# Performance work log

Hardware: AMD Instinct MI355X
Metric: run time of the kernel (lower is better)

## Reference

```python
import jax, jax.numpy as jnp
import numpy as np

# Config mirroring the TF module: cross-attention path (one_on_rna == 2),
# use_attn_augument=1, aug_multiply=0, two_d_softm=1, two_d_softm_mul_row_count=1,
# reduce_level=20 (protok used for padding masks).
B, L, D, H = 4, 1024, 512, 8
DEPTH = D // H          # 64, matches the repeat(64) in padding_to_zeros
NEG = -1.0e9


def setup_inputs() -> dict:
    key = jax.random.key(0)
    ks = jax.random.split(key, 16)
    s = np.float32(1.0 / np.sqrt(D))  # glorot-ish scale
    q = jax.random.normal(ks[0], (B, L, D), jnp.float32)
    kv = jax.random.normal(ks[1], (B, L, D), jnp.float32)
    # protein tokens; 0 == padding (compared against 0.0 in the TF code)
    protok = jax.random.randint(ks[2], (B, L), 0, 21).astype(jnp.float32)
    statpot_hb = jax.random.uniform(ks[3], (B, L, L), dtype=jnp.float32)
    statpot_pi = jax.random.uniform(ks[4], (B, L, L), dtype=jnp.float32)
    # cross padding mask: 1.0 where the protein (query) position is padding
    pad = (protok == 0.0).astype(jnp.float32)            # [B, L]
    cross_mask = jnp.broadcast_to(pad[:, :, None], (B, L, L)).astype(jnp.float32)
    wq = jax.random.normal(ks[5], (D, D), jnp.float32) * s
    wk = jax.random.normal(ks[6], (D, D), jnp.float32) * s
    wv = jax.random.normal(ks[7], (D, D), jnp.float32) * s
    wo = jax.random.normal(ks[8], (D, D), jnp.float32) * s
    bq = jnp.zeros((D,), jnp.float32)
    bk = jnp.zeros((D,), jnp.float32)
    bv = jnp.zeros((D,), jnp.float32)
    bo = jnp.zeros((D,), jnp.float32)
    aug_weight_att = jnp.ones((1,), jnp.float32)
    aug_weight_aug = jnp.ones((1,), jnp.float32)
    return dict(q=q, kv=kv, protok=protok, statpot_hb=statpot_hb,
                statpot_pi=statpot_pi, cross_mask=cross_mask,
                wq=wq, bq=bq, wk=wk, bk=bk, wv=wv, bv=bv, wo=wo, bo=bo,
                aug_weight_att=aug_weight_att, aug_weight_aug=aug_weight_aug)


def _split_heads(x):
    # [B, L, D] -> [B, H, L, depth]
    return x.reshape(B, L, H, DEPTH).transpose(0, 2, 1, 3)


def reference(q, kv, protok, statpot_hb, statpot_pi, cross_mask,
              wq, bq, wk, bk, wv, bv, wo, bo, aug_weight_att, aug_weight_aug):
    # padding_to_zeros: zero features at padded protein positions
    pad_keep = (protok != 0.0).astype(q.dtype)[:, :, None]   # [B, L, 1]
    qp = (q @ wq + bq) * pad_keep   # query side is the protein (len == max_pro_len)
    k = kv @ wk + bk
    v = kv @ wv + bv
    qh, kh, vh = _split_heads(qp), _split_heads(k), _split_heads(v)

    # unscaled QK^T (original does NOT divide by sqrt(depth))
    logits = jnp.einsum('bhqd,bhkd->bhqk', qh, kh)           # [B,H,L,L]

    # statistical-potential augmentation (aug_multiply == 0 -> additive)
    table = jnp.stack([statpot_hb, statpot_pi], axis=1)      # [B,2,L,L]
    table = jnp.repeat(table, H // 2, axis=1)                # [B,H,L,L]
    logits = logits / jnp.max(logits)
    logits = aug_weight_att * logits
    table = aug_weight_aug * table
    table = table / jnp.max(table)
    logits = logits + table

    # additive large-negative mask, broadcast over heads
    logits = logits + cross_mask[:, None, :, :] * NEG

    # 2D softmax jointly over (query, key) axes
    attn = jax.nn.softmax(logits.reshape(B, H, L * L), axis=-1).reshape(B, H, L, L)

    # rescale by number of non-padded protein rows (two_d_softm_mul_row_count)
    mul = jnp.count_nonzero(protok, axis=1).astype(attn.dtype)[:, None, None, None]
    attn = attn * mul
    attn = attn / jnp.max(attn)

    # output = attn^T @ v : contracts the QUERY axis (as in the original matmul)
    out = jnp.einsum('bhqk,bhqd->bhkd', attn, vh)            # [B,H,L,depth]
    out = out.transpose(0, 2, 1, 3).reshape(B, L, D)
    out = out @ wo + bo
    out = out * pad_keep                                     # final padding zeroing
    return out
```

## Files before the change

kernel.cpp:

```cpp
#include <hip/hip_runtime.h>
#include <math.h>

#define BB 4
#define LL 1024
#define DD 512
#define HH 8
#define DEP 64
#define NEGV (-1.0e9f)

typedef __attribute__((ext_vector_type(8))) short bf16x8;
typedef __attribute__((ext_vector_type(4))) float f32x4;
typedef unsigned short u16;
typedef unsigned int u32;

#define S_TMAX 1
#define S_TMIN 2
#define S_MUL  4
#define S_SUM  8
#define S_M    40
#define P_TMAX 128
#define P_TMIN 384
#define P_GMAX 640
#define SCAL_F 1792
#define PER_T  (BB*HH*LL*DEP)

__device__ inline u16 f2b(float x) {
  u32 u = __float_as_uint(x);
  return (u16)((u + 0x7FFFu + ((u >> 16) & 1u)) >> 16);
}
__device__ inline float b2f(u16 h) { return __uint_as_float(((u32)h) << 16); }

__device__ inline void atomicMaxF(float* addr, float val) {
  unsigned int* ua = (unsigned int*)addr;
  unsigned int old = *ua;
  while (__uint_as_float(old) < val) {
    unsigned int assumed = old;
    old = atomicCAS(ua, assumed, __float_as_uint(val));
    if (old == assumed) break;
  }
}

__global__ __launch_bounds__(256) void k_tminmax(const float* __restrict__ hb,
                                                 const float* __restrict__ pi,
                                                 const float* __restrict__ protok,
                                                 float* __restrict__ ws) {
  const int t = threadIdx.x;
  if (blockIdx.x == 4 && t < 32) {
    ws[S_SUM + t] = 0.0f; ws[S_M + t] = -INFINITY;
  }
  if (blockIdx.x < 4) {
    int b = blockIdx.x;
    int cnt = 0;
    for (int l = t; l < LL; l += 256)
      cnt += (protok[b*LL + l] != 0.0f) ? 1 : 0;
    __shared__ int shc[4];
    int lane = t & 63, w = t >> 6;
    #pragma unroll
    for (int o = 32; o > 0; o >>= 1) cnt += __shfl_down(cnt, o);
    if (lane == 0) shc[w] = cnt;
    __syncthreads();
    if (t == 0) ws[S_MUL + b] = (float)(shc[0] + shc[1] + shc[2] + shc[3]);
  }
  const int g = blockIdx.x*256 + t;
  float mx = -INFINITY, mn = INFINITY;
  #pragma unroll
  for (int rep = 0; rep < 4; ++rep) {
    float4 a[4], c[4];
    #pragma unroll
    for (int j = 0; j < 4; ++j) {
      size_t idx = (size_t)rep*262144 + (size_t)j*65536 + g;
      a[j] = ((const float4*)hb)[idx];
      c[j] = ((const float4*)pi)[idx];
    }
    #pragma unroll
    for (int j = 0; j < 4; ++j) {
      mx = fmaxf(mx, fmaxf(fmaxf(a[j].x, a[j].y), fmaxf(a[j].z, a[j].w)));
      mx = fmaxf(mx, fmaxf(fmaxf(c[j].x, c[j].y), fmaxf(c[j].z, c[j].w)));
      mn = fminf(mn, fminf(fminf(a[j].x, a[j].y), fminf(a[j].z, a[j].w)));
      mn = fminf(mn, fminf(fminf(c[j].x, c[j].y), fminf(c[j].z, c[j].w)));
    }
  }
  __shared__ float shx[4], shn[4];
  int lane = t & 63, w = t >> 6;
  #pragma unroll
  for (int o = 32; o > 0; o >>= 1) {
    mx = fmaxf(mx, __shfl_down(mx, o));
    mn = fminf(mn, __shfl_down(mn, o));
  }
  if (lane == 0) { shx[w] = mx; shn[w] = mn; }
  __syncthreads();
  if (t == 0) {
    ws[P_TMAX + blockIdx.x] = fmaxf(fmaxf(shx[0], shx[1]), fmaxf(shx[2], shx[3]));
    ws[P_TMIN + blockIdx.x] = fminf(fminf(shn[0], shn[1]), fminf(shn[2], shn[3]));
  }
}

__global__ __launch_bounds__(256) void k_prep(
    const float* __restrict__ q, const float* __restrict__ kv,
    const float* __restrict__ wq, const float* __restrict__ wk,
    const float* __restrict__ wv, const float* __restrict__ wo,
    u16* __restrict__ Xb, u16* __restrict__ WTb, float* __restrict__ ws) {
  const int bid = blockIdx.x;
  const int t = threadIdx.x;
  if (bid < 2048) {
    int tg = bid*256 + t;
    int which = tg >> 18;
    size_t off8 = (size_t)(tg & 262143) * 8;
    const float* s = which ? kv : q;
    float4 f0 = *(const float4*)&s[off8];
    float4 f1 = *(const float4*)&s[off8 + 4];
    u32 p0 = (u32)f2b(f0.x) | ((u32)f2b(f0.y) << 16);
    u32 p1 = (u32)f2b(f0.z) | ((u32)f2b(f0.w) << 16);
    u32 p2 = (u32)f2b(f1.x) | ((u32)f2b(f1.y) << 16);
    u32 p3 = (u32)f2b(f1.z) | ((u32)f2b(f1.w) << 16);
    *(int4*)&Xb[(size_t)which*PER_T + off8] = make_int4(p0, p1, p2, p3);
  } else if (bid < 2304) {
    const int wid = bid - 2048;
    const int g = wid >> 6, rem = wid & 63;
    const int k0 = (rem >> 3)*64, n0 = (rem & 7)*64;
    const float* W = (g==0)?wq:(g==1)?wk:(g==2)?wv:wo;
    __shared__ u16 Ls[64][72];
    {
      const int r = t>>2, c16 = (t&3)*16;
      float v[16];
      #pragma unroll
      for (int j=0;j<4;++j) {
        float4 f = *(const float4*)&W[(size_t)(k0+r)*DD + n0 + c16 + 4*j];
        v[4*j]=f.x; v[4*j+1]=f.y; v[4*j+2]=f.z; v[4*j+3]=f.w;
      }
      u32 pk_[8];
      #pragma unroll
      for (int j=0;j<8;++j) pk_[j] = (u32)f2b(v[2*j]) | ((u32)f2b(v[2*j+1])<<16);
      *(int4*)&Ls[r][c16]   = make_int4(pk_[0],pk_[1],pk_[2],pk_[3]);
      *(int4*)&Ls[r][c16+8] = make_int4(pk_[4],pk_[5],pk_[6],pk_[7]);
    }
    __syncthreads();
    {
      const int n = t>>2, kk = (t&3)*16;
      u16 u[16];
      #pragma unroll
      for (int j=0;j<16;++j) u[j] = Ls[kk+j][n];
      u32 q_[8];
      #pragma unroll
      for (int j=0;j<8;++j) q_[j] = (u32)u[2*j] | ((u32)u[2*j+1]<<16);
      size_t dst = ((size_t)(g*DD + n0 + n))*DD + k0 + kk;
      *(int4*)&WTb[dst]   = make_int4(q_[0],q_[1],q_[2],q_[3]);
      *(int4*)&WTb[dst+8] = make_int4(q_[4],q_[5],q_[6],q_[7]);
    }
  } else {
    float tm = ws[P_TMAX + t];
    float tn = ws[P_TMIN + t];
    __shared__ float st[4], sn[4];
    int lane = t & 63, w = t >> 6;
    #pragma unroll
    for (int o = 32; o > 0; o >>= 1) {
      tm = fmaxf(tm, __shfl_down(tm, o));
      tn = fminf(tn, __shfl_down(tn, o));
    }
    if (lane == 0) { st[w] = tm; sn[w] = tn; }
    __syncthreads();
    if (t == 0) {
      ws[S_TMAX] = fmaxf(fmaxf(st[0], st[1]), fmaxf(st[2], st[3]));
      ws[S_TMIN] = fminf(fminf(sn[0], sn[1]), fminf(sn[2], sn[3]));
    }
  }
}

__global__ __launch_bounds__(256) void k1_proj(
    const float* __restrict__ protok,
    const float* __restrict__ bq, const float* __restrict__ bk,
    const float* __restrict__ bv,
    const u16* __restrict__ Xb, const u16* __restrict__ WTb,
    u16* __restrict__ QPb, u16* __restrict__ KHb, u16* __restrict__ VTb) {
  const int gid = blockIdx.z;
  const u16* X = Xb + (gid == 0 ? 0 : (size_t)PER_T);
  const float* bia = (gid == 0) ? bq : (gid == 1) ? bk : bv;
  const int m0 = blockIdx.x*64;
  const int h  = blockIdx.y;
  __shared__ u16 As[64][72];
  __shared__ u16 Bs[64][72];
  const int t = threadIdx.x;
  const int w = t>>6, lane = t&63, i = lane&15, g2 = lane>>4;
  const int sr = t>>2, sc = (t&3)*16;

  f32x4 acc[4];
  #pragma unroll
  for (int ct=0;ct<4;++ct) acc[ct] = (f32x4){0.f,0.f,0.f,0.f};

  for (int kk0 = 0; kk0 < DD; kk0 += 64) {
    __syncthreads();
    {
      size_t sx = (size_t)(m0+sr)*DD + kk0 + sc;
      *(int4*)&As[sr][sc]   = *(const int4*)&X[sx];
      *(int4*)&As[sr][sc+8] = *(const int4*)&X[sx+8];
    }
    {
      size_t src = ((size_t)(gid*DD + h*64 + sr))*DD + kk0 + sc;
      *(int4*)&Bs[sr][sc]   = *(const int4*)&WTb[src];
      *(int4*)&Bs[sr][sc+8] = *(const int4*)&WTb[src+8];
    }
    __syncthreads();
    bf16x8 a0 = *(const bf16x8*)&As[16*w + i][g2*8];
    bf16x8 a1 = *(const bf16x8*)&As[16*w + i][32 + g2*8];
    #pragma unroll
    for (int ct=0; ct<4; ++ct) {
      bf16x8 b0 = *(const bf16x8*)&Bs[ct*16 + i][g2*8];
      bf16x8 b1 = *(const bf16x8*)&Bs[ct*16 + i][32 + g2*8];
      acc[ct] = __builtin_amdgcn_mfma_f32_16x16x32_bf16(a0, b0, acc[ct], 0,0,0);
      acc[ct] = __builtin_amdgcn_mfma_f32_16x16x32_bf16(a1, b1, acc[ct], 0,0,0);
    }
  }
  __syncthreads();
  const int lrow = 16*w + g2*4;
  if (gid == 2) {
    #pragma unroll
    for (int ct=0;ct<4;++ct)
      #pragma unroll
      for (int r=0;r<4;++r)
        As[lrow + r][ct*16 + i] = f2b(acc[ct][r] + bia[h*64 + ct*16 + i]);
    __syncthreads();
    const int b = m0 >> 10, l0 = m0 & 1023;
    const int d = t>>2, lc = (t&3)*16;
    u16 u[16];
    #pragma unroll
    for (int j=0;j<16;++j) u[j] = As[lc+j][d];
    u32 q_[8];
    #pragma unroll
    for (int j=0;j<8;++j) q_[j] = (u32)u[2*j] | ((u32)u[2*j+1]<<16);
    size_t dst = ((size_t)(b*HH + h)*DEP + d)*LL + l0 + lc;
    *(int4*)&VTb[dst]   = make_int4(q_[0],q_[1],q_[2],q_[3]);
    *(int4*)&VTb[dst+8] = make_int4(q_[4],q_[5],q_[6],q_[7]);
  } else {
    u16* Y = (gid == 0) ? QPb : KHb;
    #pragma unroll
    for (int ct=0;ct<4;++ct)
      #pragma unroll
      for (int r=0;r<4;++r) {
        int m = m0 + lrow + r;
        float keep = (gid == 0) ? ((protok[m] != 0.0f) ? 1.0f : 0.0f) : 1.0f;
        int b = m >> 10, l = m & 1023;
        float val = (acc[ct][r] + bia[h*64 + ct*16 + i]) * keep;
        Y[((size_t)(b*HH + h)*LL + l)*DEP + ct*16 + i] = f2b(val);
      }
  }
}

__global__ __launch_bounds__(256) void k3_gmax(
    const u16* __restrict__ QPb, const u16* __restrict__ KHb,
    float* __restrict__ wsf) {
  const int q0 = blockIdx.x*128, bh = blockIdx.y, kz = blockIdx.z;
  __shared__ u16 Qs[2][64][72];
  __shared__ u16 Ks[2][64][72];
  const int t = threadIdx.x;
  const int w = t>>6, lane = t&63, i = lane&15, g2 = lane>>4;
  const int sr = t>>2, sc = (t&3)*16;
  const u16* Qb = QPb + (size_t)bh*LL*DEP;
  const u16* Kb = KHb + (size_t)bh*LL*DEP;
  #pragma unroll
  for (int qs = 0; qs < 2; ++qs) {
    size_t sq = (size_t)(q0 + qs*64 + sr)*DEP + sc;
    *(int4*)&Qs[qs][sr][sc]   = *(const int4*)&Qb[sq];
    *(int4*)&Qs[qs][sr][sc+8] = *(const int4*)&Qb[sq+8];
  }
  const int kb = kz*4;
  int4 rn0 = *(const int4*)&Kb[(size_t)(kb*64 + sr)*DEP + sc];
  int4 rn1 = *(const int4*)&Kb[(size_t)(kb*64 + sr)*DEP + sc + 8];
  __syncthreads();
  *(int4*)&Ks[0][sr][sc]   = rn0;
  *(int4*)&Ks[0][sr][sc+8] = rn1;
  rn0 = *(const int4*)&Kb[(size_t)((kb+1)*64 + sr)*DEP + sc];
  rn1 = *(const int4*)&Kb[(size_t)((kb+1)*64 + sr)*DEP + sc + 8];
  __syncthreads();
  bf16x8 a0[2], a1[2];
  #pragma unroll
  for (int qs = 0; qs < 2; ++qs) {
    a0[qs] = *(const bf16x8*)&Qs[qs][16*w + i][g2*8];
    a1[qs] = *(const bf16x8*)&Qs[qs][16*w + i][32 + g2*8];
  }
  float mx = -INFINITY;
  for (int kt = 0; kt < 4; ++kt) {
    const int cur = kt & 1;
    #pragma unroll
    for (int ct=0;ct<4;++ct) {
      bf16x8 b0 = *(const bf16x8*)&Ks[cur][ct*16 + i][g2*8];
      bf16x8 b1 = *(const bf16x8*)&Ks[cur][ct*16 + i][32 + g2*8];
      #pragma unroll
      for (int qs=0;qs<2;++qs) {
        f32x4 z = (f32x4){0.f,0.f,0.f,0.f};
        z = __builtin_amdgcn_mfma_f32_16x16x32_bf16(a0[qs], b0, z, 0,0,0);
        z = __builtin_amdgcn_mfma_f32_16x16x32_bf16(a1[qs], b1, z, 0,0,0);
        mx = fmaxf(mx, fmaxf(fmaxf(z[0],z[1]), fmaxf(z[2],z[3])));
      }
    }
    if (kt < 3) {
      __syncthreads();
      *(int4*)&Ks[cur^1][sr][sc]   = rn0;
      *(int4*)&Ks[cur^1][sr][sc+8] = rn1;
      if (kt < 2) {
        rn0 = *(const int4*)&Kb[(size_t)((kb+kt+2)*64 + sr)*DEP + sc];
        rn1 = *(const int4*)&Kb[(size_t)((kb+kt+2)*64 + sr)*DEP + sc + 8];
      }
      __syncthreads();
    }
  }
  __shared__ float red[4];
  #pragma unroll
  for (int o = 32; o > 0; o >>= 1) mx = fmaxf(mx, __shfl_down(mx, o));
  if (lane == 0) red[w] = mx;
  __syncthreads();
  if (t == 0)
    wsf[P_GMAX + (bh*8 + blockIdx.x)*4 + kz] =
        fmaxf(fmaxf(red[0],red[1]), fmaxf(red[2],red[3]));
}

__global__ __launch_bounds__(256) void k4_fused(
    const float* __restrict__ protok,
    const float* __restrict__ hb, const float* __restrict__ pi,
    const float* __restrict__ w_att, const float* __restrict__ w_aug,
    const u16* __restrict__ QPb, const u16* __restrict__ KHb,
    const u16* __restrict__ VTb,
    u16* __restrict__ Ob0, u16* __restrict__ Ob1,
    float* __restrict__ wsf) {
  const int k0 = blockIdx.x*64;
  const int bh = blockIdx.y, b = bh>>3, h = bh&7;
  const int qbase = blockIdx.z * 512;
  u16* Obz = blockIdx.z ? Ob1 : Ob0;
  const float* tab = ((h < 4) ? hb : pi) + (size_t)b*LL*LL;
  const int t = threadIdx.x;
  const int w = t>>6, lane = t&63, i = lane&15, g2 = lane>>4;
  const int sr = t>>2, sc = (t&3)*16;
  const int qlb = 16*w + g2*4;

  __shared__ float gsh;
  {
    float gm = -INFINITY;
    #pragma unroll
    for (int j=0;j<4;++j) gm = fmaxf(gm, wsf[P_GMAX + j*256 + t]);
    __shared__ float red[4];
    #pragma unroll
    for (int o = 32; o > 0; o >>= 1) gm = fmaxf(gm, __shfl_down(gm, o));
    if (lane == 0) red[w] = gm;
    __syncthreads();
    if (t == 0) gsh = fmaxf(fmaxf(red[0],red[1]), fmaxf(red[2],red[3]));
  }
  const float tmaxr = wsf[S_TMAX], tminr = wsf[S_TMIN];
  const float wa = w_att[0], wg = w_aug[0];
  const float tden = (wg >= 0.0f) ? (wg * tmaxr) : (wg * tminr);
  const float inv_t = wg / tden;

  __shared__ u16 Ks[64][72];
  __shared__ u16 Qs[64][72];
  __shared__ u16 Vt[64][72];
  __shared__ u16 Pt[64][72];
  {
    size_t sk = ((size_t)bh*LL + k0 + sr)*DEP + sc;
    *(int4*)&Ks[sr][sc]   = *(const int4*)&KHb[sk];
    *(int4*)&Ks[sr][sc+8] = *(const int4*)&KHb[sk+8];
  }
  int4 rq0 = *(const int4*)&QPb[((size_t)bh*LL + qbase + sr)*DEP + sc];
  int4 rq1 = *(const int4*)&QPb[((size_t)bh*LL + qbase + sr)*DEP + sc + 8];
  int4 rv0 = *(const int4*)&VTb[((size_t)bh*DEP + sr)*LL + qbase + sc];
  int4 rv1 = *(const int4*)&VTb[((size_t)bh*DEP + sr)*LL + qbase + sc + 8];
  float tvr[4][4];
  #pragma unroll
  for (int r=0;r<4;++r)
    #pragma unroll
    for (int ct=0;ct<4;++ct)
      tvr[r][ct] = tab[(size_t)(qbase + qlb + r)*LL + k0 + ct*16 + i];
  __syncthreads();
  const float inv_g = wa / gsh;
  bf16x8 kb0[4], kb1[4];
  #pragma unroll
  for (int ct=0;ct<4;++ct) {
    kb0[ct] = *(const bf16x8*)&Ks[ct*16 + i][g2*8];
    kb1[ct] = *(const bf16x8*)&Ks[ct*16 + i][32 + g2*8];
  }
  f32x4 accO[4];
  #pragma unroll
  for (int dt=0;dt<4;++dt) accO[dt] = (f32x4){0.f,0.f,0.f,0.f};
  float lsum = 0.0f, lmax = -INFINITY;

  for (int q0 = qbase; q0 < qbase + 512; q0 += 64) {
    const bool more = (q0 + 64) < (qbase + 512);
    __syncthreads();
    *(int4*)&Qs[sr][sc]   = rq0;
    *(int4*)&Qs[sr][sc+8] = rq1;
    *(int4*)&Vt[sr][sc]   = rv0;
    *(int4*)&Vt[sr][sc+8] = rv1;
    __syncthreads();
    if (more) {
      rq0 = *(const int4*)&QPb[((size_t)bh*LL + q0 + 64 + sr)*DEP + sc];
      rq1 = *(const int4*)&QPb[((size_t)bh*LL + q0 + 64 + sr)*DEP + sc + 8];
      rv0 = *(const int4*)&VTb[((size_t)bh*DEP + sr)*LL + q0 + 64 + sc];
      rv1 = *(const int4*)&VTb[((size_t)bh*DEP + sr)*LL + q0 + 64 + sc + 8];
    }
    bf16x8 a0 = *(const bf16x8*)&Qs[16*w + i][g2*8];
    bf16x8 a1 = *(const bf16x8*)&Qs[16*w + i][32 + g2*8];
    f32x4 s4[4];
    #pragma unroll
    for (int ct=0; ct<4; ++ct) {
      f32x4 z = (f32x4){0.f,0.f,0.f,0.f};
      z = __builtin_amdgcn_mfma_f32_16x16x32_bf16(a0, kb0[ct], z, 0,0,0);
      z = __builtin_amdgcn_mfma_f32_16x16x32_bf16(a1, kb1[ct], z, 0,0,0);
      s4[ct] = z;
    }
    float tv2[4][4];
    if (more) {
      #pragma unroll
      for (int r=0;r<4;++r)
        #pragma unroll
        for (int ct=0;ct<4;++ct)
          tv2[r][ct] = tab[(size_t)(q0 + 64 + qlb + r)*LL + k0 + ct*16 + i];
    }
    float madd[4];
    #pragma unroll
    for (int r=0;r<4;++r)
      madd[r] = (protok[b*LL + q0 + qlb + r] == 0.0f) ? NEGV : 0.0f;
    #pragma unroll
    for (int ct=0;ct<4;++ct) {
      float pr[4];
      #pragma unroll
      for (int r=0;r<4;++r) {
        float sp = fmaf(s4[ct][r], inv_g, fmaf(tvr[r][ct], inv_t, madd[r]));
        lmax = fmaxf(lmax, sp);
        float p = __expf(sp);
        lsum += p;
        pr[r] = p;
      }
      u32 pk0 = (u32)f2b(pr[0]) | ((u32)f2b(pr[1])<<16);
      u32 pk1 = (u32)f2b(pr[2]) | ((u32)f2b(pr[3])<<16);
      *(uint2*)&Pt[ct*16 + i][qlb] = make_uint2(pk0, pk1);
    }
    __syncthreads();
    bf16x8 pa0 = *(const bf16x8*)&Pt[16*w + i][g2*8];
    bf16x8 pa1 = *(const bf16x8*)&Pt[16*w + i][32 + g2*8];
    #pragma unroll
    for (int dt=0; dt<4; ++dt) {
      bf16x8 v0 = *(const bf16x8*)&Vt[dt*16 + i][g2*8];
      bf16x8 v1 = *(const bf16x8*)&Vt[dt*16 + i][32 + g2*8];
      accO[dt] = __builtin_amdgcn_mfma_f32_16x16x32_bf16(pa0, v0, accO[dt], 0,0,0);
      accO[dt] = __builtin_amdgcn_mfma_f32_16x16x32_bf16(pa1, v1, accO[dt], 0,0,0);
    }
    if (more) {
      #pragma unroll
      for (int r=0;r<4;++r)
        #pragma unroll
        for (int ct=0;ct<4;++ct) tvr[r][ct] = tv2[r][ct];
    }
  }
  #pragma unroll
  for (int dt=0;dt<4;++dt)
    #pragma unroll
    for (int r=0;r<4;++r)
      Obz[((size_t)bh*LL + k0 + qlb + r)*DEP + dt*16 + i] = f2b(accO[dt][r]);
  __shared__ float rs[4], rm[4];
  #pragma unroll
  for (int o = 32; o > 0; o >>= 1) {
    lsum += __shfl_down(lsum, o);
    lmax = fmaxf(lmax, __shfl_down(lmax, o));
  }
  if (lane == 0) { rs[w] = lsum; rm[w] = lmax; }
  __syncthreads();
  if (t == 0) {
    atomicAdd(&wsf[S_SUM + bh], rs[0]+rs[1]+rs[2]+rs[3]);
    atomicMaxF(&wsf[S_M + bh], fmaxf(fmaxf(rm[0], rm[1]), fmaxf(rm[2], rm[3])));
  }
}

__global__ __launch_bounds__(256) void k5_out(
    const float* __restrict__ protok,
    const float* __restrict__ bo,
    const u16* __restrict__ WTb,
    const u16* __restrict__ O0, const u16* __restrict__ O1,
    const float* __restrict__ wsf, float* __restrict__ out) {
  const int m0 = blockIdx.x*64, n0 = blockIdx.y*64;
  const int b = m0 >> 10, l0 = m0 & 1023;
  __shared__ u16 As[64][72];
  __shared__ u16 Bs[64][72];
  __shared__ float csh[8];
  const int t = threadIdx.x;
  const int w = t>>6, lane = t&63, i = lane&15, g2 = lane>>4;
  const int sr = t>>2, sc = (t&3)*16;

  __shared__ float ash[32];
  if (t < 32)
    ash[t] = wsf[S_MUL + (t>>3)] * __expf(wsf[S_M + t]) / wsf[S_SUM + t];
  __syncthreads();
  if (t < 8) {
    float amax = -INFINITY;
    #pragma unroll
    for (int j = 0; j < 32; ++j) amax = fmaxf(amax, ash[j]);
    csh[t] = (wsf[S_MUL + b] / wsf[S_SUM + b*HH + t]) / amax;
  }

  f32x4 acc[4];
  #pragma unroll
  for (int ct=0;ct<4;++ct) acc[ct] = (f32x4){0.f,0.f,0.f,0.f};

  for (int kk0 = 0; kk0 < DD; kk0 += 64) {
    const int h = kk0 >> 6;
    __syncthreads();
    {
      union { int4 v[2]; u16 u[16]; } u0, u1;
      size_t so = ((size_t)(b*HH + h)*LL + l0 + sr)*DEP + sc;
      u0.v[0] = *(const int4*)&O0[so];
      u0.v[1] = *(const int4*)&O0[so+8];
      u1.v[0] = *(const int4*)&O1[so];
      u1.v[1] = *(const int4*)&O1[so+8];
      const float cs = csh[h];
      u32 pk_[8];
      #pragma unroll
      for (int j=0;j<8;++j) {
        float lo = (b2f(u0.u[2*j])   + b2f(u1.u[2*j]))   * cs;
        float hi = (b2f(u0.u[2*j+1]) + b2f(u1.u[2*j+1])) * cs;
        pk_[j] = (u32)f2b(lo) | ((u32)f2b(hi)<<16);
      }
      *(int4*)&As[sr][sc]   = make_int4(pk_[0],pk_[1],pk_[2],pk_[3]);
      *(int4*)&As[sr][sc+8] = make_int4(pk_[4],pk_[5],pk_[6],pk_[7]);
    }
    {
      size_t src = ((size_t)(3*DD + n0 + sr))*DD + kk0 + sc;
      *(int4*)&Bs[sr][sc]   = *(const int4*)&WTb[src];
      *(int4*)&Bs[sr][sc+8] = *(const int4*)&WTb[src+8];
    }
    __syncthreads();
    bf16x8 a0 = *(const bf16x8*)&As[16*w + i][g2*8];
    bf16x8 a1 = *(const bf16x8*)&As[16*w + i][32 + g2*8];
    #pragma unroll
    for (int ct=0; ct<4; ++ct) {
      bf16x8 b0 = *(const bf16x8*)&Bs[ct*16 + i][g2*8];
      bf16x8 b1 = *(const bf16x8*)&Bs[ct*16 + i][32 + g2*8];
      acc[ct] = __builtin_amdgcn_mfma_f32_16x16x32_bf16(a0, b0, acc[ct], 0,0,0);
      acc[ct] = __builtin_amdgcn_mfma_f32_16x16x32_bf16(a1, b1, acc[ct], 0,0,0);
    }
  }
  #pragma unroll
  for (int ct=0;ct<4;++ct)
    #pragma unroll
    for (int r=0;r<4;++r) {
      int m = m0 + 16*w + g2*4 + r;
      float keep = (protok[m] != 0.0f) ? 1.0f : 0.0f;
      out[(size_t)m*DD + n0 + ct*16 + i] = (acc[ct][r] + bo[n0 + ct*16 + i]) * keep;
    }
}

extern "C" void kernel_launch(void* const* d_in, const int* in_sizes, int n_in,
                              void* d_out, int out_size, void* d_ws, size_t ws_size,
                              hipStream_t stream) {
  const float* q      = (const float*)d_in[0];
  const float* kv     = (const float*)d_in[1];
  const float* protok = (const float*)d_in[2];
  const float* hb     = (const float*)d_in[3];
  const float* pi     = (const float*)d_in[4];
  const float* wq = (const float*)d_in[6];
  const float* bq = (const float*)d_in[7];
  const float* wk = (const float*)d_in[8];
  const float* bk = (const float*)d_in[9];
  const float* wv = (const float*)d_in[10];
  const float* bv = (const float*)d_in[11];
  const float* wo = (const float*)d_in[12];
  const float* bo = (const float*)d_in[13];
  const float* w_att = (const float*)d_in[14];
  const float* w_aug = (const float*)d_in[15];
  float* wsf = (float*)d_ws;
  float* out = (float*)d_out;

  u16* base = (u16*)(wsf + SCAL_F);
  u16* QPb = base;
  u16* KHb = QPb + PER_T;
  u16* VTb = KHb + PER_T;
  u16* XO  = VTb + PER_T;
  u16* WTb = XO  + 2*PER_T;
  u16* Xb  = XO;
  u16* Ob0 = XO;
  u16* Ob1 = XO + PER_T;

  k_tminmax <<<256, 256, 0, stream>>>(hb, pi, protok, wsf);
  k_prep    <<<2305, 256, 0, stream>>>(q, kv, wq, wk, wv, wo, Xb, WTb, wsf);
  k1_proj   <<<dim3(64, 8, 3), 256, 0, stream>>>(protok, bq, bk, bv, Xb, WTb, QPb, KHb, VTb);
  k3_gmax   <<<dim3(8, 32, 4), 256, 0, stream>>>(QPb, KHb, wsf);
  k4_fused  <<<dim3(16, 32, 2), 256, 0, stream>>>(protok, hb, pi, w_att, w_aug,
                                                  QPb, KHb, VTb, Ob0, Ob1, wsf);
  k5_out    <<<dim3(64, 8), 256, 0, stream>>>(protok, bo, WTb, Ob0, Ob1, wsf, out);
}
```

Measured before the change: 215.3 us.

## Fold table min/max into prep kernel and process full query range per attention block

Moves the statpot min/max reduction and the row-count into extra blocks of the prep kernel, which removes one launch. The final table min/max reduction now happens inside the attention kernel. The attention kernel drops the query-axis split (z=2), so each block walks all 1024 queries in 128-row steps and produces a single output buffer. That removes the partial-output sum in the projection kernel. It also keeps Q fragments in registers, caches the padding mask in LDS, and processes two 64-row subtiles per iteration for more MFMA work per sync. The cost is half the attention grid (512 blocks), which may lower occupancy and latency hiding, plus higher register pressure.

```diff
diff --git a/kernel.cpp b/kernel.cpp
--- a/kernel.cpp
+++ b/kernel.cpp
@@ -40,65 +40,12 @@
   }
 }
 
-__global__ __launch_bounds__(256) void k_tminmax(const float* __restrict__ hb,
-                                                 const float* __restrict__ pi,
-                                                 const float* __restrict__ protok,
-                                                 float* __restrict__ ws) {
-  const int t = threadIdx.x;
-  if (blockIdx.x == 4 && t < 32) {
-    ws[S_SUM + t] = 0.0f; ws[S_M + t] = -INFINITY;
-  }
-  if (blockIdx.x < 4) {
-    int b = blockIdx.x;
-    int cnt = 0;
-    for (int l = t; l < LL; l += 256)
-      cnt += (protok[b*LL + l] != 0.0f) ? 1 : 0;
-    __shared__ int shc[4];
-    int lane = t & 63, w = t >> 6;
-    #pragma unroll
-    for (int o = 32; o > 0; o >>= 1) cnt += __shfl_down(cnt, o);
-    if (lane == 0) shc[w] = cnt;
-    __syncthreads();
-    if (t == 0) ws[S_MUL + b] = (float)(shc[0] + shc[1] + shc[2] + shc[3]);
-  }
-  const int g = blockIdx.x*256 + t;
-  float mx = -INFINITY, mn = INFINITY;
-  #pragma unroll
-  for (int rep = 0; rep < 4; ++rep) {
-    float4 a[4], c[4];
-    #pragma unroll
-    for (int j = 0; j < 4; ++j) {
-      size_t idx = (size_t)rep*262144 + (size_t)j*65536 + g;
-      a[j] = ((const float4*)hb)[idx];
-      c[j] = ((const float4*)pi)[idx];
-    }
-    #pragma unroll
-    for (int j = 0; j < 4; ++j) {
-      mx = fmaxf(mx, fmaxf(fmaxf(a[j].x, a[j].y), fmaxf(a[j].z, a[j].w)));
-      mx = fmaxf(mx, fmaxf(fmaxf(c[j].x, c[j].y), fmaxf(c[j].z, c[j].w)));
-      mn = fminf(mn, fminf(fminf(a[j].x, a[j].y), fminf(a[j].z, a[j].w)));
-      mn = fminf(mn, fminf(fminf(c[j].x, c[j].y), fminf(c[j].z, c[j].w)));
-    }
-  }
-  __shared__ float shx[4], shn[4];
-  int lane = t & 63, w = t >> 6;
-  #pragma unroll
-  for (int o = 32; o > 0; o >>= 1) {
-    mx = fmaxf(mx, __shfl_down(mx, o));
-    mn = fminf(mn, __shfl_down(mn, o));
-  }
-  if (lane == 0) { shx[w] = mx; shn[w] = mn; }
-  __syncthreads();
-  if (t == 0) {
-    ws[P_TMAX + blockIdx.x] = fmaxf(fmaxf(shx[0], shx[1]), fmaxf(shx[2], shx[3]));
-    ws[P_TMIN + blockIdx.x] = fminf(fminf(shn[0], shn[1]), fminf(shn[2], shn[3]));
-  }
-}
-
 __global__ __launch_bounds__(256) void k_prep(
     const float* __restrict__ q, const float* __restrict__ kv,
     const float* __restrict__ wq, const float* __restrict__ wk,
     const float* __restrict__ wv, const float* __restrict__ wo,
+    const float* __restrict__ hb, const float* __restrict__ pi,
+    const float* __restrict__ protok,
     u16* __restrict__ Xb, u16* __restrict__ WTb, float* __restrict__ ws) {
   const int bid = blockIdx.x;
   const int t = threadIdx.x;
@@ -147,22 +94,53 @@
       *(int4*)&WTb[dst]   = make_int4(q_[0],q_[1],q_[2],q_[3]);
       *(int4*)&WTb[dst+8] = make_int4(q_[4],q_[5],q_[6],q_[7]);
     }
+  } else if (bid < 2560) {
+    const int g = (bid - 2304)*256 + t;
+    float mx = -INFINITY, mn = INFINITY;
+    #pragma unroll
+    for (int rep = 0; rep < 4; ++rep) {
+      float4 a[4], c[4];
+      #pragma unroll
+      for (int j = 0; j < 4; ++j) {
+        size_t idx = (size_t)rep*262144 + (size_t)j*65536 + g;
+        a[j] = ((const float4*)hb)[idx];
+        c[j] = ((const float4*)pi)[idx];
+      }
+      #pragma unroll
+      for (int j = 0; j < 4; ++j) {
+        mx = fmaxf(mx, fmaxf(fmaxf(a[j].x, a[j].y), fmaxf(a[j].z, a[j].w)));
+        mx = fmaxf(mx, fmaxf(fmaxf(c[j].x, c[j].y), fmaxf(c[j].z, c[j].w)));
+        mn = fminf(mn, fminf(fminf(a[j].x, a[j].y), fminf(a[j].z, a[j].w)));
+        mn = fminf(mn, fminf(fminf(c[j].x, c[j].y), fminf(c[j].z, c[j].w)));
+      }
+    }
+    __shared__ float shx[4], shn[4];
+    int lane = t & 63, w = t >> 6;
+    #pragma unroll
+    for (int o = 32; o > 0; o >>= 1) {
+      mx = fmaxf(mx, __shfl_down(mx, o));
+      mn = fminf(mn, __shfl_down(mn, o));
+    }
+    if (lane == 0) { shx[w] = mx; shn[w] = mn; }
+    __syncthreads();
+    if (t == 0) {
+      ws[P_TMAX + bid - 2304] = fmaxf(fmaxf(shx[0], shx[1]), fmaxf(shx[2], shx[3]));
+      ws[P_TMIN + bid - 2304] = fminf(fminf(shn[0], shn[1]), fminf(shn[2], shn[3]));
+    }
+  } else if (bid < 2564) {
+    int b = bid - 2560;
+    int cnt = 0;
+    for (int l = t; l < LL; l += 256)
+      cnt += (protok[b*LL + l] != 0.0f) ? 1 : 0;
+    __shared__ int shc[4];
+    int lane = t & 63, w = t >> 6;
+    #pragma unroll
+    for (int o = 32; o > 0; o >>= 1) cnt += __shfl_down(cnt, o);
+    if (lane == 0) shc[w] = cnt;
+    __syncthreads();
+    if (t == 0) ws[S_MUL + b] = (float)(shc[0] + shc[1] + shc[2] + shc[3]);
   } else {
-    float tm = ws[P_TMAX + t];
-    float tn = ws[P_TMIN + t];
-    __shared__ float st[4], sn[4];
-    int lane = t & 63, w = t >> 6;
-    #pragma unroll
-    for (int o = 32; o > 0; o >>= 1) {
-      tm = fmaxf(tm, __shfl_down(tm, o));
-      tn = fminf(tn, __shfl_down(tn, o));
-    }
-    if (lane == 0) { st[w] = tm; sn[w] = tn; }
-    __syncthreads();
-    if (t == 0) {
-      ws[S_TMAX] = fmaxf(fmaxf(st[0], st[1]), fmaxf(st[2], st[3]));
-      ws[S_TMIN] = fminf(fminf(sn[0], sn[1]), fminf(sn[2], sn[3]));
-    }
+    if (t < 32) { ws[S_SUM + t] = 0.0f; ws[S_M + t] = -INFINITY; }
   }
 }
 
@@ -318,57 +296,71 @@
     const float* __restrict__ hb, const float* __restrict__ pi,
     const float* __restrict__ w_att, const float* __restrict__ w_aug,
     const u16* __restrict__ QPb, const u16* __restrict__ KHb,
-    const u16* __restrict__ VTb,
-    u16* __restrict__ Ob0, u16* __restrict__ Ob1,
+    const u16* __restrict__ VTb, u16* __restrict__ Ob,
     float* __restrict__ wsf) {
   const int k0 = blockIdx.x*64;
   const int bh = blockIdx.y, b = bh>>3, h = bh&7;
-  const int qbase = blockIdx.z * 512;
-  u16* Obz = blockIdx.z ? Ob1 : Ob0;
   const float* tab = ((h < 4) ? hb : pi) + (size_t)b*LL*LL;
   const int t = threadIdx.x;
   const int w = t>>6, lane = t&63, i = lane&15, g2 = lane>>4;
   const int sr = t>>2, sc = (t&3)*16;
   const int qlb = 16*w + g2*4;
 
-  __shared__ float gsh;
+  __shared__ u16 Ks[64][72];
+  __shared__ u16 Vt[2][64][72];
+  __shared__ u16 Pt[2][64][72];
+  __shared__ float Msk[1024];
+  __shared__ float rg[4], rt[4], rn[4];
+
   {
     float gm = -INFINITY;
     #pragma unroll
     for (int j=0;j<4;++j) gm = fmaxf(gm, wsf[P_GMAX + j*256 + t]);
-    __shared__ float red[4];
-    #pragma unroll
-    for (int o = 32; o > 0; o >>= 1) gm = fmaxf(gm, __shfl_down(gm, o));
-    if (lane == 0) red[w] = gm;
-    __syncthreads();
-    if (t == 0) gsh = fmaxf(fmaxf(red[0],red[1]), fmaxf(red[2],red[3]));
-  }
-  const float tmaxr = wsf[S_TMAX], tminr = wsf[S_TMIN];
-  const float wa = w_att[0], wg = w_aug[0];
-  const float tden = (wg >= 0.0f) ? (wg * tmaxr) : (wg * tminr);
-  const float inv_t = wg / tden;
-
-  __shared__ u16 Ks[64][72];
-  __shared__ u16 Qs[64][72];
-  __shared__ u16 Vt[64][72];
-  __shared__ u16 Pt[64][72];
+    float tm = wsf[P_TMAX + t], tn = wsf[P_TMIN + t];
+    #pragma unroll
+    for (int o = 32; o > 0; o >>= 1) {
+      gm = fmaxf(gm, __shfl_down(gm, o));
+      tm = fmaxf(tm, __shfl_down(tm, o));
+      tn = fminf(tn, __shfl_down(tn, o));
+    }
+    if (lane == 0) { rg[w] = gm; rt[w] = tm; rn[w] = tn; }
+  }
+  #pragma unroll
+  for (int j=0;j<4;++j) {
+    int l = j*256 + t;
+    Msk[l] = (protok[b*LL + l] == 0.0f) ? NEGV : 0.0f;
+  }
   {
     size_t sk = ((size_t)bh*LL + k0 + sr)*DEP + sc;
     *(int4*)&Ks[sr][sc]   = *(const int4*)&KHb[sk];
     *(int4*)&Ks[sr][sc+8] = *(const int4*)&KHb[sk+8];
   }
-  int4 rq0 = *(const int4*)&QPb[((size_t)bh*LL + qbase + sr)*DEP + sc];
-  int4 rq1 = *(const int4*)&QPb[((size_t)bh*LL + qbase + sr)*DEP + sc + 8];
-  int4 rv0 = *(const int4*)&VTb[((size_t)bh*DEP + sr)*LL + qbase + sc];
-  int4 rv1 = *(const int4*)&VTb[((size_t)bh*DEP + sr)*LL + qbase + sc + 8];
-  float tvr[4][4];
+  const u16* Qbase = QPb + (size_t)bh*LL*DEP;
+  const u16* Vbase = VTb + (size_t)bh*DEP*LL;
+  bf16x8 aqA0 = *(const bf16x8*)&Qbase[(size_t)(16*w+i)*DEP + g2*8];
+  bf16x8 aqA1 = *(const bf16x8*)&Qbase[(size_t)(16*w+i)*DEP + 32 + g2*8];
+  bf16x8 aqB0 = *(const bf16x8*)&Qbase[(size_t)(64+16*w+i)*DEP + g2*8];
+  bf16x8 aqB1 = *(const bf16x8*)&Qbase[(size_t)(64+16*w+i)*DEP + 32 + g2*8];
+  int4 rvA0 = *(const int4*)&Vbase[(size_t)sr*LL + sc];
+  int4 rvA1 = *(const int4*)&Vbase[(size_t)sr*LL + sc + 8];
+  int4 rvB0 = *(const int4*)&Vbase[(size_t)sr*LL + 64 + sc];
+  int4 rvB1 = *(const int4*)&Vbase[(size_t)sr*LL + 64 + sc + 8];
+  float tvA[4][4], tvB[4][4];
   #pragma unroll
   for (int r=0;r<4;++r)
     #pragma unroll
-    for (int ct=0;ct<4;++ct)
-      tvr[r][ct] = tab[(size_t)(qbase + qlb + r)*LL + k0 + ct*16 + i];
-  __syncthreads();
-  const float inv_g = wa / gsh;
+    for (int ct=0;ct<4;++ct) {
+      tvA[r][ct] = tab[(size_t)(qlb + r)*LL + k0 + ct*16 + i];
+      tvB[r][ct] = tab[(size_t)(64 + qlb + r)*LL + k0 + ct*16 + i];
+    }
+  __syncthreads();
+  const float gmax  = fmaxf(fmaxf(rg[0],rg[1]), fmaxf(rg[2],rg[3]));
+  const float tmaxr = fmaxf(fmaxf(rt[0],rt[1]), fmaxf(rt[2],rt[3]));
+  const float tminr = fminf(fminf(rn[0],rn[1]), fminf(rn[2],rn[3]));
+  const float wa = w_att[0], wg = w_aug[0];
+  const float inv_g = wa / gmax;
+  const float tden  = (wg >= 0.0f) ? (wg * tmaxr) : (wg * tminr);
+  const float inv_t = wg / tden;
   bf16x8 kb0[4], kb1[4];
   #pragma unroll
   for (int ct=0;ct<4;++ct) {
@@ -380,79 +372,101 @@
   for (int dt=0;dt<4;++dt) accO[dt] = (f32x4){0.f,0.f,0.f,0.f};
   float lsum = 0.0f, lmax = -INFINITY;
 
-  for (int q0 = qbase; q0 < qbase + 512; q0 += 64) {
-    const bool more = (q0 + 64) < (qbase + 512);
-    __syncthreads();
-    *(int4*)&Qs[sr][sc]   = rq0;
-    *(int4*)&Qs[sr][sc+8] = rq1;
-    *(int4*)&Vt[sr][sc]   = rv0;
-    *(int4*)&Vt[sr][sc+8] = rv1;
-    __syncthreads();
+  for (int q0 = 0; q0 < LL; q0 += 128) {
+    const bool more = (q0 + 128) < LL;
+    __syncthreads();
+    *(int4*)&Vt[0][sr][sc]   = rvA0;
+    *(int4*)&Vt[0][sr][sc+8] = rvA1;
+    *(int4*)&Vt[1][sr][sc]   = rvB0;
+    *(int4*)&Vt[1][sr][sc+8] = rvB1;
+    __syncthreads();
+    bf16x8 aqA0n, aqA1n, aqB0n, aqB1n;
     if (more) {
-      rq0 = *(const int4*)&QPb[((size_t)bh*LL + q0 + 64 + sr)*DEP + sc];
-      rq1 = *(const int4*)&QPb[((size_t)bh*LL + q0 + 64 + sr)*DEP + sc + 8];
-      rv0 = *(const int4*)&VTb[((size_t)bh*DEP + sr)*LL + q0 + 64 + sc];
-      rv1 = *(const int4*)&VTb[((size_t)bh*DEP + sr)*LL + q0 + 64 + sc + 8];
-    }
-    bf16x8 a0 = *(const bf16x8*)&Qs[16*w + i][g2*8];
-    bf16x8 a1 = *(const bf16x8*)&Qs[16*w + i][32 + g2*8];
-    f32x4 s4[4];
+      rvA0 = *(const int4*)&Vbase[(size_t)sr*LL + q0 + 128 + sc];
+      rvA1 = *(const int4*)&Vbase[(size_t)sr*LL + q0 + 128 + sc + 8];
+      rvB0 = *(const int4*)&Vbase[(size_t)sr*LL + q0 + 192 + sc];
+      rvB1 = *(const int4*)&Vbase[(size_t)sr*LL + q0 + 192 + sc + 8];
+      aqA0n = *(const bf16x8*)&Qbase[(size_t)(q0+128+16*w+i)*DEP + g2*8];
+      aqA1n = *(const bf16x8*)&Qbase[(size_t)(q0+128+16*w+i)*DEP + 32 + g2*8];
+      aqB0n = *(const bf16x8*)&Qbase[(size_t)(q0+192+16*w+i)*DEP + g2*8];
+      aqB1n = *(const bf16x8*)&Qbase[(size_t)(q0+192+16*w+i)*DEP + 32 + g2*8];
+    }
+    f32x4 sA[4], sB[4];
     #pragma unroll
     for (int ct=0; ct<4; ++ct) {
-      f32x4 z = (f32x4){0.f,0.f,0.f,0.f};
-      z = __builtin_amdgcn_mfma_f32_16x16x32_bf16(a0, kb0[ct], z, 0,0,0);
-      z = __builtin_amdgcn_mfma_f32_16x16x32_bf16(a1, kb1[ct], z, 0,0,0);
-      s4[ct] = z;
-    }
-    float tv2[4][4];
+      f32x4 zA = (f32x4){0.f,0.f,0.f,0.f};
+      zA = __builtin_amdgcn_mfma_f32_16x16x32_bf16(aqA0, kb0[ct], zA, 0,0,0);
+      zA = __builtin_amdgcn_mfma_f32_16x16x32_bf16(aqA1, kb1[ct], zA, 0,0,0);
+      sA[ct] = zA;
+      f32x4 zB = (f32x4){0.f,0.f,0.f,0.f};
+      zB = __builtin_amdgcn_mfma_f32_16x16x32_bf16(aqB0, kb0[ct], zB, 0,0,0);
+      zB = __builtin_amdgcn_mfma_f32_16x16x32_bf16(aqB1, kb1[ct], zB, 0,0,0);
+      sB[ct] = zB;
+    }
+    float t2A[4][4], t2B[4][4];
     if (more) {
       #pragma unroll
       for (int r=0;r<4;++r)
         #pragma unroll
-        for (int ct=0;ct<4;++ct)
-          tv2[r][ct] = tab[(size_t)(q0 + 64 + qlb + r)*LL + k0 + ct*16 + i];
-    }
-    float madd[4];
-    #pragma unroll
-    for (int r=0;r<4;++r)
-      madd[r] = (protok[b*LL + q0 + qlb + r] == 0.0f) ? NEGV : 0.0f;
+        for (int ct=0;ct<4;++ct) {
+          t2A[r][ct] = tab[(size_t)(q0 + 128 + qlb + r)*LL + k0 + ct*16 + i];
+          t2B[r][ct] = tab[(size_t)(q0 + 192 + qlb + r)*LL + k0 + ct*16 + i];
+        }
+    }
+    float mA[4], mB[4];
+    #pragma unroll
+    for (int r=0;r<4;++r) {
+      mA[r] = Msk[q0 + qlb + r];
+      mB[r] = Msk[q0 + 64 + qlb + r];
+    }
     #pragma unroll
     for (int ct=0;ct<4;++ct) {
-      float pr[4];
+      float pA[4], pB[4];
       #pragma unroll
       for (int r=0;r<4;++r) {
-        float sp = fmaf(s4[ct][r], inv_g, fmaf(tvr[r][ct], inv_t, madd[r]));
-        lmax = fmaxf(lmax, sp);
-        float p = __expf(sp);
-        lsum += p;
-        pr[r] = p;
-      }
-      u32 pk0 = (u32)f2b(pr[0]) | ((u32)f2b(pr[1])<<16);
-      u32 pk1 = (u32)f2b(pr[2]) | ((u32)f2b(pr[3])<<16);
-      *(uint2*)&Pt[ct*16 + i][qlb] = make_uint2(pk0, pk1);
-    }
-    __syncthreads();
-    bf16x8 pa0 = *(const bf16x8*)&Pt[16*w + i][g2*8];
-    bf16x8 pa1 = *(const bf16x8*)&Pt[16*w + i][32 + g2*8];
+        float spA = fmaf(sA[ct][r], inv_g, fmaf(tvA[r][ct], inv_t, mA[r]));
+        float spB = fmaf(sB[ct][r], inv_g, fmaf(tvB[r][ct], inv_t, mB[r]));
+        lmax = fmaxf(lmax, fmaxf(spA, spB));
+        pA[r] = __expf(spA);
+        pB[r] = __expf(spB);
+        lsum += pA[r] + pB[r];
+      }
+      *(uint2*)&Pt[0][ct*16 + i][qlb] =
+          make_uint2((u32)f2b(pA[0]) | ((u32)f2b(pA[1])<<16),
+                     (u32)f2b(pA[2]) | ((u32)f2b(pA[3])<<16));
+      *(uint2*)&Pt[1][ct*16 + i][qlb] =
+          make_uint2((u32)f2b(pB[0]) | ((u32)f2b(pB[1])<<16),
+                     (u32)f2b(pB[2]) | ((u32)f2b(pB[3])<<16));
+    }
+    __syncthreads();
+    bf16x8 paA0 = *(const bf16x8*)&Pt[0][16*w + i][g2*8];
+    bf16x8 paA1 = *(const bf16x8*)&Pt[0][16*w + i][32 + g2*8];
+    bf16x8 paB0 = *(const bf16x8*)&Pt[1][16*w + i][g2*8];
+    bf16x8 paB1 = *(const bf16x8*)&Pt[1][16*w + i][32 + g2*8];
     #pragma unroll
     for (int dt=0; dt<4; ++dt) {
-      bf16x8 v0 = *(const bf16x8*)&Vt[dt*16 + i][g2*8];
-      bf16x8 v1 = *(const bf16x8*)&Vt[dt*16 + i][32 + g2*8];
-      accO[dt] = __builtin_amdgcn_mfma_f32_16x16x32_bf16(pa0, v0, accO[dt], 0,0,0);
-      accO[dt] = __builtin_amdgcn_mfma_f32_16x16x32_bf16(pa1, v1, accO[dt], 0,0,0);
+      bf16x8 vA0 = *(const bf16x8*)&Vt[0][dt*16 + i][g2*8];
+      bf16x8 vA1 = *(const bf16x8*)&Vt[0][dt*16 + i][32 + g2*8];
+      accO[dt] = __builtin_amdgcn_mfma_f32_16x16x32_bf16(paA0, vA0, accO[dt], 0,0,0);
+      accO[dt] = __builtin_amdgcn_mfma_f32_16x16x32_bf16(paA1, vA1, accO[dt], 0,0,0);
+      bf16x8 vB0 = *(const bf16x8*)&Vt[1][dt*16 + i][g2*8];
+      bf16x8 vB1 = *(const bf16x8*)&Vt[1][dt*16 + i][32 + g2*8];
+      accO[dt] = __builtin_amdgcn_mfma_f32_16x16x32_bf16(paB0, vB0, accO[dt], 0,0,0);
+      accO[dt] = __builtin_amdgcn_mfma_f32_16x16x32_bf16(paB1, vB1, accO[dt], 0,0,0);
     }
     if (more) {
+      aqA0 = aqA0n; aqA1 = aqA1n; aqB0 = aqB0n; aqB1 = aqB1n;
       #pragma unroll
       for (int r=0;r<4;++r)
         #pragma unroll
-        for (int ct=0;ct<4;++ct) tvr[r][ct] = tv2[r][ct];
+        for (int ct=0;ct<4;++ct) { tvA[r][ct] = t2A[r][ct]; tvB[r][ct] = t2B[r][ct]; }
     }
   }
   #pragma unroll
   for (int dt=0;dt<4;++dt)
     #pragma unroll
     for (int r=0;r<4;++r)
-      Obz[((size_t)bh*LL + k0 + qlb + r)*DEP + dt*16 + i] = f2b(accO[dt][r]);
+      Ob[((size_t)bh*LL + k0 + qlb + r)*DEP + dt*16 + i] = f2b(accO[dt][r]);
   __shared__ float rs[4], rm[4];
   #pragma unroll
   for (int o = 32; o > 0; o >>= 1) {
@@ -470,8 +484,7 @@
 __global__ __launch_bounds__(256) void k5_out(
     const float* __restrict__ protok,
     const float* __restrict__ bo,
-    const u16* __restrict__ WTb,
-    const u16* __restrict__ O0, const u16* __restrict__ O1,
+    const u16* __restrict__ WTb, const u16* __restrict__ Ob,
     const float* __restrict__ wsf, float* __restrict__ out) {
   const int m0 = blockIdx.x*64, n0 = blockIdx.y*64;
   const int b = m0 >> 10, l0 = m0 & 1023;
@@ -501,20 +514,15 @@
     const int h = kk0 >> 6;
     __syncthreads();
     {
-      union { int4 v[2]; u16 u[16]; } u0, u1;
+      union { int4 v[2]; u16 u[16]; } uu;
       size_t so = ((size_t)(b*HH + h)*LL + l0 + sr)*DEP + sc;
-      u0.v[0] = *(const int4*)&O0[so];
-      u0.v[1] = *(const int4*)&O0[so+8];
-      u1.v[0] = *(const int4*)&O1[so];
-      u1.v[1] = *(const int4*)&O1[so+8];
+      uu.v[0] = *(const int4*)&Ob[so];
+      uu.v[1] = *(const int4*)&Ob[so+8];
       const float cs = csh[h];
       u32 pk_[8];
       #pragma unroll
-      for (int j=0;j<8;++j) {
-        float lo = (b2f(u0.u[2*j])   + b2f(u1.u[2*j]))   * cs;
-        float hi = (b2f(u0.u[2*j+1]) + b2f(u1.u[2*j+1])) * cs;
-        pk_[j] = (u32)f2b(lo) | ((u32)f2b(hi)<<16);
-      }
+      for (int j=0;j<8;++j)
+        pk_[j] = (u32)f2b(b2f(uu.u[2*j])*cs) | ((u32)f2b(b2f(uu.u[2*j+1])*cs)<<16);
       *(int4*)&As[sr][sc]   = make_int4(pk_[0],pk_[1],pk_[2],pk_[3]);
       *(int4*)&As[sr][sc+8] = make_int4(pk_[4],pk_[5],pk_[6],pk_[7]);
     }
@@ -572,14 +580,14 @@
   u16* XO  = VTb + PER_T;
   u16* WTb = XO  + 2*PER_T;
   u16* Xb  = XO;
-  u16* Ob0 = XO;
-  u16* Ob1 = XO + PER_T;
-
-  k_tminmax <<<256, 256, 0, stream>>>(hb, pi, protok, wsf);
-  k_prep    <<<2305, 256, 0, stream>>>(q, kv, wq, wk, wv, wo, Xb, WTb, wsf);
-  k1_proj   <<<dim3(64, 8, 3), 256, 0, stream>>>(protok, bq, bk, bv, Xb, WTb, QPb, KHb, VTb);
-  k3_gmax   <<<dim3(8, 32, 4), 256, 0, stream>>>(QPb, KHb, wsf);
-  k4_fused  <<<dim3(16, 32, 2), 256, 0, stream>>>(protok, hb, pi, w_att, w_aug,
-                                                  QPb, KHb, VTb, Ob0, Ob1, wsf);
-  k5_out    <<<dim3(64, 8), 256, 0, stream>>>(protok, bo, WTb, Ob0, Ob1, wsf, out);
-}
+  u16* Ob  = XO;
+
+  k_prep  <<<2565, 256, 0, stream>>>(q, kv, wq, wk, wv, wo, hb, pi, protok,
+                                     Xb, WTb, wsf);
+  k1_proj <<<dim3(64, 8, 3), 256, 0, stream>>>(protok, bq, bk, bv, Xb, WTb,
+                                               QPb, KHb, VTb);
+  k3_gmax <<<dim3(8, 32, 4), 256, 0, stream>>>(QPb, KHb, wsf);
+  k4_fused<<<dim3(16, 32), 256, 0, stream>>>(protok, hb, pi, w_att, w_aug,
+                                             QPb, KHb, VTb, Ob, wsf);
+  k5_out  <<<dim3(64, 8), 256, 0, stream>>>(protok, bo, WTb, Ob, wsf, out);
+}
```

Result: faster. 208.4 us (-3.2%).
